# Kernel tuning notes

Hardware: AMD Instinct MI355X
Metric: run time of the kernel (lower is better)

The kernel has to match this reference:

```python
import jax, jax.numpy as jnp
import numpy as np

N_NODES = 40000
N_EDGES = 640000
EMB = 128
OUT_EMB = 256
NUM_DENSE = 3
NUM_TARGETS = 12
NUM_RADIAL = 6


def setup_inputs() -> dict:
    key = jax.random.key(0)
    ks = jax.random.split(key, 8)
    n_atoms = jax.random.normal(ks[0], (N_NODES, EMB), dtype=jnp.float32)
    x = jax.random.normal(ks[1], (N_EDGES, EMB), dtype=jnp.float32)
    rbf = jax.random.normal(ks[2], (N_EDGES, NUM_RADIAL), dtype=jnp.float32)
    idnb_i = jax.random.randint(ks[3], (N_EDGES,), 0, N_NODES, dtype=jnp.int64 if jax.config.read('jax_enable_x64') else jnp.int32)
    s = 0.05
    W_rbf = jax.random.normal(ks[4], (NUM_RADIAL, EMB), dtype=jnp.float32) * s
    W_up = jax.random.normal(ks[5], (EMB, OUT_EMB), dtype=jnp.float32) * s
    W_mlp = jax.random.normal(ks[6], (NUM_DENSE, OUT_EMB, OUT_EMB), dtype=jnp.float32) * s
    b_mlp = jnp.zeros((NUM_DENSE, OUT_EMB), dtype=jnp.float32)
    W_final = jax.random.normal(ks[7], (OUT_EMB, NUM_TARGETS), dtype=jnp.float32) * s
    return {"n_atoms": n_atoms, "x": x, "rbf": rbf, "idnb_i": idnb_i,
            "W_rbf": W_rbf, "W_up": W_up, "W_mlp": W_mlp, "b_mlp": b_mlp,
            "W_final": W_final}


def reference(n_atoms, x, rbf, idnb_i, W_rbf, W_up, W_mlp, b_mlp, W_final):
    # g = Dense(emb_size, no bias)(rbf): [M, EMB]
    g = rbf @ W_rbf
    # elementwise edge gate
    xe = g * x                                  # [M, EMB]
    # scatter-sum edges -> nodes (pooling_method='sum')
    pooled = jax.ops.segment_sum(xe, idnb_i, num_segments=n_atoms.shape[0])  # [N, EMB]
    # up-projection, no bias
    h = pooled @ W_up                           # [N, OUT_EMB]
    # GraphMLP: num_dense layers, swish activation, with bias
    for i in range(W_mlp.shape[0]):
        h = jax.nn.silu(h @ W_mlp[i] + b_mlp[i])
    # final output projection, no bias
    return h @ W_final                          # [N, NUM_TARGETS]
```

## Files before the change

kernel.cpp:

```cpp
#include <hip/hip_runtime.h>
#include <hip/hip_fp16.h>
#include <math.h>

constexpr int kNodes   = 40000;
constexpr int kEdges   = 640000;
constexpr int kEmb     = 128;
constexpr int kOut     = 256;
constexpr int kTargets = 12;
constexpr int kRadial  = 6;

typedef float        f32x4 __attribute__((ext_vector_type(4)));
typedef unsigned int u32x4 __attribute__((ext_vector_type(4)));

__device__ __forceinline__ unsigned short f2h(float f) {
  return __half_as_ushort(__float2half(f));
}
__device__ __forceinline__ void mfma_f16(f32x4& c, u32x4 a, u32x4 b) {
  asm volatile("v_mfma_f32_16x16x32_f16 %0, %1, %2, %0" : "+v"(c) : "v"(a), "v"(b));
}

__global__ __launch_bounds__(256) void zero_counts(int* __restrict__ c) {
  const int i = blockIdx.x * 256 + threadIdx.x;
  if (i < kNodes) c[i] = 0;
}

__global__ __launch_bounds__(256) void hist_kernel(const int* __restrict__ idnb,
                                                   int* __restrict__ counts) {
  const int e = blockIdx.x * 256 + threadIdx.x;
  if (e < kEdges) atomicAdd(&counts[idnb[e]], 1);
}

__global__ __launch_bounds__(256) void scan_pass1(const int* __restrict__ counts,
                                                  int* __restrict__ bsum) {
  __shared__ int sm[256];
  const int idx = blockIdx.x * 256 + threadIdx.x;
  sm[threadIdx.x] = (idx < kNodes) ? counts[idx] : 0;
  __syncthreads();
  for (int d = 128; d > 0; d >>= 1) {
    if (threadIdx.x < d) sm[threadIdx.x] += sm[threadIdx.x + d];
    __syncthreads();
  }
  if (threadIdx.x == 0) bsum[blockIdx.x] = sm[0];
}

__global__ __launch_bounds__(256) void scan_pass3(const int* __restrict__ counts,
                                                  const int* __restrict__ bsum,
                                                  int* __restrict__ offs,
                                                  int* __restrict__ next,
                                                  int nblk) {
  __shared__ int sm[256];
  __shared__ int base;
  const int t = threadIdx.x;
  sm[t] = (t < nblk && t < (int)blockIdx.x) ? bsum[t] : 0;
  __syncthreads();
  for (int d = 128; d > 0; d >>= 1) {
    if (t < d) sm[t] += sm[t + d];
    __syncthreads();
  }
  if (t == 0) base = sm[0];
  __syncthreads();

  const int idx = blockIdx.x * 256 + t;
  const int v = (idx < kNodes) ? counts[idx] : 0;
  sm[t] = v;
  __syncthreads();
  for (int d = 1; d < 256; d <<= 1) {
    const int xsh = (t >= d) ? sm[t - d] : 0;
    __syncthreads();
    sm[t] += xsh;
    __syncthreads();
  }
  if (idx < kNodes) {
    const int e = base + sm[t] - v;
    offs[idx] = e;
    next[idx] = e;
  }
  if (blockIdx.x == 0 && t == 0) offs[kNodes] = kEdges;
}

__global__ __launch_bounds__(256) void fill_kernel(const int* __restrict__ idnb,
                                                   int* __restrict__ next,
                                                   int* __restrict__ edgeIdx) {
  const int e = blockIdx.x * 256 + threadIdx.x;
  if (e < kEdges) {
    const int p = atomicAdd(&next[idnb[e]], 1);
    edgeIdx[p] = e;
  }
}

__global__ __launch_bounds__(256) void prep_weights(
    const float* __restrict__ Wup, const float* __restrict__ Wmlp,
    const float* __restrict__ Wfin,
    unsigned short* __restrict__ WtUp, unsigned short* __restrict__ WtM,
    unsigned short* __restrict__ WtFin) {
  const int id = blockIdx.x * 256 + threadIdx.x;
  if (id < 256 * 128) {
    const int n = id >> 7, k = id & 127;
    WtUp[id] = f2h(Wup[k * 256 + n]);
    return;
  }
  const int id2 = id - 256 * 128;
  if (id2 < 3 * 256 * 256) {
    const int l = id2 >> 16, rem = id2 & 65535, n = rem >> 8, k = rem & 255;
    WtM[id2] = f2h(Wmlp[l * 65536 + k * 256 + n]);
    return;
  }
  const int id3 = id2 - 3 * 256 * 256;
  if (id3 < 16 * 256) {
    const int n = id3 >> 8, k = id3 & 255;
    WtFin[id3] = (n < kTargets) ? f2h(Wfin[k * kTargets + n]) : (unsigned short)0;
  }
}

__global__ __launch_bounds__(256) void gather_kernel(
    const float* __restrict__ x, const float* __restrict__ rbf,
    const int* __restrict__ offs, const int* __restrict__ edgeIdx,
    const float* __restrict__ W_rbf, unsigned short* __restrict__ pooled) {
  __shared__ float wLds[kRadial * kEmb];
  for (int i = threadIdx.x; i < kRadial * kEmb; i += 256) wLds[i] = W_rbf[i];
  __syncthreads();

  const int sub = threadIdx.x & 31;
  const int n   = blockIdx.x * 8 + (threadIdx.x >> 5);

  float4 w[kRadial];
#pragma unroll
  for (int j = 0; j < kRadial; ++j)
    w[j] = *(const float4*)(wLds + j * kEmb + sub * 4);

  const int beg = offs[n], end = offs[n + 1];
  float4 acc = make_float4(0.f, 0.f, 0.f, 0.f);

  if (beg < end) {
    int e = edgeIdx[beg];
    float4 xv = *(const float4*)(x + (size_t)e * kEmb + sub * 4);
    const float* rr = rbf + (size_t)e * kRadial;
    float2 ra = *(const float2*)(rr);
    float2 rb = *(const float2*)(rr + 2);
    float2 rc = *(const float2*)(rr + 4);

    for (int i = beg; i < end; ++i) {
      float4 xv_n;
      float2 na, nb, nc;
      const bool more = (i + 1 < end);
      if (more) {
        const int en = edgeIdx[i + 1];
        xv_n = *(const float4*)(x + (size_t)en * kEmb + sub * 4);
        const float* rn = rbf + (size_t)en * kRadial;
        na = *(const float2*)(rn);
        nb = *(const float2*)(rn + 2);
        nc = *(const float2*)(rn + 4);
      }
      float4 g;
      g.x = ra.x * w[0].x + ra.y * w[1].x + rb.x * w[2].x + rb.y * w[3].x +
            rc.x * w[4].x + rc.y * w[5].x;
      g.y = ra.x * w[0].y + ra.y * w[1].y + rb.x * w[2].y + rb.y * w[3].y +
            rc.x * w[4].y + rc.y * w[5].y;
      g.z = ra.x * w[0].z + ra.y * w[1].z + rb.x * w[2].z + rb.y * w[3].z +
            rc.x * w[4].z + rc.y * w[5].z;
      g.w = ra.x * w[0].w + ra.y * w[1].w + rb.x * w[2].w + rb.y * w[3].w +
            rc.x * w[4].w + rc.y * w[5].w;
      acc.x += g.x * xv.x;
      acc.y += g.y * xv.y;
      acc.z += g.z * xv.z;
      acc.w += g.w * xv.w;
      if (more) {
        xv = xv_n;
        ra = na; rb = nb; rc = nc;
      }
    }
  }
  ushort4 hv;
  hv.x = f2h(acc.x);
  hv.y = f2h(acc.y);
  hv.z = f2h(acc.z);
  hv.w = f2h(acc.w);
  *(ushort4*)(pooled + (size_t)n * kEmb + sub * 4) = hv;
}

__global__ __launch_bounds__(256) void fused_mlp(
    const unsigned short* __restrict__ pooled,
    const unsigned short* __restrict__ WtUp,
    const unsigned short* __restrict__ WtM,
    const unsigned short* __restrict__ WtFin,
    const float* __restrict__ b_mlp, float* __restrict__ out) {
  __shared__ unsigned short act[64][266];
  __shared__ unsigned short sB[2][256][40];

  const int tid     = threadIdx.x;
  const int rowBase = blockIdx.x * 64;
  const int w    = tid >> 6;
  const int lane = tid & 63;
  const int lrow = lane & 15;
  const int kgrp = lane >> 4;

#pragma unroll
  for (int p = 0; p < 4; ++p) {
    const int q = p * 256 + tid;
    const int r = q >> 4, c = q & 15;
    *(u32x4*)&act[r][c * 8] =
        *(const u32x4*)(pooled + (size_t)(rowBase + r) * kEmb + c * 8);
  }
  __syncthreads();

  for (int l = 0; l < 4; ++l) {
    const int K = (l == 0) ? 128 : 256;
    const int nc = K >> 5;
    const unsigned short* W = (l == 0) ? WtUp : WtM + (size_t)(l - 1) * 65536;

#pragma unroll
    for (int p = 0; p < 4; ++p) {
      const int q = p * 256 + tid;
      const int n = q >> 2, c4 = q & 3;
      *(u32x4*)&sB[0][n][c4 * 8] = *(const u32x4*)(W + (size_t)n * K + c4 * 8);
    }
    __syncthreads();

    f32x4 acc[4][4];
#pragma unroll
    for (int i = 0; i < 4; ++i)
#pragma unroll
      for (int j = 0; j < 4; ++j) acc[i][j] = f32x4{0.f, 0.f, 0.f, 0.f};

    for (int c = 0; c < nc; ++c) {
      if (c + 1 < nc) {
        const int kb = (c + 1) * 32;
#pragma unroll
        for (int p = 0; p < 4; ++p) {
          const int q = p * 256 + tid;
          const int n = q >> 2, c4 = q & 3;
          *(u32x4*)&sB[(c + 1) & 1][n][c4 * 8] =
              *(const u32x4*)(W + (size_t)n * K + kb + c4 * 8);
        }
      }
      u32x4 a[4];
#pragma unroll
      for (int i = 0; i < 4; ++i)
        a[i] = *(const u32x4*)&act[i * 16 + lrow][c * 32 + kgrp * 8];
#pragma unroll
      for (int j = 0; j < 4; ++j) {
        const u32x4 b = *(const u32x4*)&sB[c & 1][w * 64 + j * 16 + lrow][kgrp * 8];
#pragma unroll
        for (int i = 0; i < 4; ++i) mfma_f16(acc[i][j], a[i], b);
      }
      __syncthreads();
    }

    const float* bias = (l >= 1) ? b_mlp + (size_t)(l - 1) * kOut : nullptr;
#pragma unroll
    for (int j = 0; j < 4; ++j) {
      const int col = w * 64 + j * 16 + lrow;
      const float bj = (l >= 1) ? bias[col] : 0.f;
#pragma unroll
      for (int i = 0; i < 4; ++i) {
#pragma unroll
        for (int r = 0; r < 4; ++r) {
          float v = acc[i][j][r];
          if (l >= 1) {
            v += bj;
            v = v / (1.f + __expf(-v));
          }
          act[i * 16 + kgrp * 4 + r][col] = f2h(v);
        }
      }
    }
    __syncthreads();
  }

  unsigned short (*sWf)[266] = (unsigned short(*)[266]) & sB[0][0][0];
  float (*sPart)[64][17]     = (float(*)[64][17]) & sB[1][0][0];
#pragma unroll
  for (int p = 0; p < 2; ++p) {
    const int q = p * 256 + tid;
    const int n = q >> 5, c = q & 31;
    *(u32x4*)&sWf[n][c * 8] = *(const u32x4*)(WtFin + (size_t)n * 256 + c * 8);
  }
  __syncthreads();

  f32x4 accF[4];
#pragma unroll
  for (int i = 0; i < 4; ++i) accF[i] = f32x4{0.f, 0.f, 0.f, 0.f};
#pragma unroll
  for (int s = 0; s < 2; ++s) {
    const int cc = w * 2 + s;
    const u32x4 b = *(const u32x4*)&sWf[lrow][cc * 32 + kgrp * 8];
#pragma unroll
    for (int i = 0; i < 4; ++i) {
      const u32x4 a = *(const u32x4*)&act[i * 16 + lrow][cc * 32 + kgrp * 8];
      mfma_f16(accF[i], a, b);
    }
  }
#pragma unroll
  for (int i = 0; i < 4; ++i)
#pragma unroll
    for (int r = 0; r < 4; ++r)
      sPart[w][i * 16 + kgrp * 4 + r][lrow] = accF[i][r];
  __syncthreads();

  for (int q = tid; q < 64 * kTargets; q += 256) {
    const int r = q / kTargets, t = q % kTargets;
    out[(size_t)(rowBase + r) * kTargets + t] =
        sPart[0][r][t] + sPart[1][r][t] + sPart[2][r][t] + sPart[3][r][t];
  }
}

extern "C" void kernel_launch(void* const* d_in, const int* in_sizes, int n_in,
                              void* d_out, int out_size, void* d_ws, size_t ws_size,
                              hipStream_t stream) {
  const float* x      = (const float*)d_in[1];
  const float* rbf    = (const float*)d_in[2];
  const int*   idnb   = (const int*)d_in[3];
  const float* W_rbf  = (const float*)d_in[4];
  const float* W_up   = (const float*)d_in[5];
  const float* W_mlp  = (const float*)d_in[6];
  const float* b_mlp  = (const float*)d_in[7];
  const float* W_fin  = (const float*)d_in[8];
  float* out = (float*)d_out;

  char* wp = (char*)d_ws;
  auto alloc = [&](size_t bytes) -> void* {
    void* r = wp;
    wp += (bytes + 255) & ~(size_t)255;
    return r;
  };
  unsigned short* pooled = (unsigned short*)alloc((size_t)kNodes * kEmb * 2);
  unsigned short* WtUp   = (unsigned short*)alloc(256 * 128 * 2);
  unsigned short* WtM    = (unsigned short*)alloc(3 * 256 * 256 * 2);
  unsigned short* WtFin  = (unsigned short*)alloc(16 * 256 * 2);
  int* counts  = (int*)alloc((size_t)kNodes * 4);
  int* offs    = (int*)alloc((size_t)(kNodes + 8) * 4);
  int* next    = (int*)alloc((size_t)kNodes * 4);
  int* edgeIdx = (int*)alloc((size_t)kEdges * 4);
  int* bsum    = (int*)alloc(256 * 4);

  constexpr int nScanBlk = (kNodes + 255) / 256;

  zero_counts<<<nScanBlk, 256, 0, stream>>>(counts);
  hist_kernel<<<kEdges / 256, 256, 0, stream>>>(idnb, counts);
  scan_pass1<<<nScanBlk, 256, 0, stream>>>(counts, bsum);
  scan_pass3<<<nScanBlk, 256, 0, stream>>>(counts, bsum, offs, next, nScanBlk);
  fill_kernel<<<kEdges / 256, 256, 0, stream>>>(idnb, next, edgeIdx);

  constexpr int prepElems = 256 * 128 + 3 * 256 * 256 + 16 * 256;
  prep_weights<<<(prepElems + 255) / 256, 256, 0, stream>>>(
      W_up, W_mlp, W_fin, WtUp, WtM, WtFin);

  gather_kernel<<<kNodes / 8, 256, 0, stream>>>(x, rbf, offs, edgeIdx, W_rbf,
                                                pooled);

  fused_mlp<<<kNodes / 64, 256, 0, stream>>>(pooled, WtUp, WtM, WtFin, b_mlp,
                                             out);
}
```

Measured before the change: 243.5 us.

## Pre-swizzle MLP weights for direct global-to-LDS loads and fold zeroing into prep

Result: faster. 221.2 us (-9.2%).

```diff
diff --git a/kernel.cpp b/kernel.cpp
--- a/kernel.cpp
+++ b/kernel.cpp
@@ -12,16 +12,14 @@
 typedef float        f32x4 __attribute__((ext_vector_type(4)));
 typedef unsigned int u32x4 __attribute__((ext_vector_type(4)));
 
+typedef __attribute__((address_space(1))) const void gvoid;
+typedef __attribute__((address_space(3))) void       lvoid;
+
 __device__ __forceinline__ unsigned short f2h(float f) {
   return __half_as_ushort(__float2half(f));
 }
 __device__ __forceinline__ void mfma_f16(f32x4& c, u32x4 a, u32x4 b) {
   asm volatile("v_mfma_f32_16x16x32_f16 %0, %1, %2, %0" : "+v"(c) : "v"(a), "v"(b));
-}
-
-__global__ __launch_bounds__(256) void zero_counts(int* __restrict__ c) {
-  const int i = blockIdx.x * 256 + threadIdx.x;
-  if (i < kNodes) c[i] = 0;
 }
 
 __global__ __launch_bounds__(256) void hist_kernel(const int* __restrict__ idnb,
@@ -92,20 +90,29 @@
     const float* __restrict__ Wup, const float* __restrict__ Wmlp,
     const float* __restrict__ Wfin,
     unsigned short* __restrict__ WtUp, unsigned short* __restrict__ WtM,
-    unsigned short* __restrict__ WtFin) {
+    unsigned short* __restrict__ WtFin, int* __restrict__ counts) {
   const int id = blockIdx.x * 256 + threadIdx.x;
-  if (id < 256 * 128) {
-    const int n = id >> 7, k = id & 127;
+  if (id < kNodes) counts[id] = 0;
+
+  if (id < 32768) {
+    const int e = id & 7, u = id >> 3;
+    const int l = u & 63, j = (u >> 6) & 3, wv = (u >> 8) & 3, c = u >> 10;
+    const int n = wv * 64 + j * 16 + (l & 15);
+    const int k = c * 32 + (l >> 4) * 8 + e;
     WtUp[id] = f2h(Wup[k * 256 + n]);
     return;
   }
-  const int id2 = id - 256 * 128;
-  if (id2 < 3 * 256 * 256) {
-    const int l = id2 >> 16, rem = id2 & 65535, n = rem >> 8, k = rem & 255;
-    WtM[id2] = f2h(Wmlp[l * 65536 + k * 256 + n]);
+  const int id2 = id - 32768;
+  if (id2 < 3 * 65536) {
+    const int L = id2 >> 16, r = id2 & 65535;
+    const int e = r & 7, u = r >> 3;
+    const int l = u & 63, j = (u >> 6) & 3, wv = (u >> 8) & 3, c = u >> 10;
+    const int n = wv * 64 + j * 16 + (l & 15);
+    const int k = c * 32 + (l >> 4) * 8 + e;
+    WtM[id2] = f2h(Wmlp[L * 65536 + k * 256 + n]);
     return;
   }
-  const int id3 = id2 - 3 * 256 * 256;
+  const int id3 = id2 - 3 * 65536;
   if (id3 < 16 * 256) {
     const int n = id3 >> 8, k = id3 & 255;
     WtFin[id3] = (n < kTargets) ? f2h(Wfin[k * kTargets + n]) : (unsigned short)0;
@@ -123,52 +130,24 @@
   const int sub = threadIdx.x & 31;
   const int n   = blockIdx.x * 8 + (threadIdx.x >> 5);
 
-  float4 w[kRadial];
+  f32x4 w[kRadial];
 #pragma unroll
   for (int j = 0; j < kRadial; ++j)
-    w[j] = *(const float4*)(wLds + j * kEmb + sub * 4);
+    w[j] = *(const f32x4*)(wLds + j * kEmb + sub * 4);
 
   const int beg = offs[n], end = offs[n + 1];
-  float4 acc = make_float4(0.f, 0.f, 0.f, 0.f);
-
-  if (beg < end) {
-    int e = edgeIdx[beg];
-    float4 xv = *(const float4*)(x + (size_t)e * kEmb + sub * 4);
+  f32x4 acc = {0.f, 0.f, 0.f, 0.f};
+
+  for (int i = beg; i < end; ++i) {
+    const int e = edgeIdx[i];
     const float* rr = rbf + (size_t)e * kRadial;
-    float2 ra = *(const float2*)(rr);
-    float2 rb = *(const float2*)(rr + 2);
-    float2 rc = *(const float2*)(rr + 4);
-
-    for (int i = beg; i < end; ++i) {
-      float4 xv_n;
-      float2 na, nb, nc;
-      const bool more = (i + 1 < end);
-      if (more) {
-        const int en = edgeIdx[i + 1];
-        xv_n = *(const float4*)(x + (size_t)en * kEmb + sub * 4);
-        const float* rn = rbf + (size_t)en * kRadial;
-        na = *(const float2*)(rn);
-        nb = *(const float2*)(rn + 2);
-        nc = *(const float2*)(rn + 4);
-      }
-      float4 g;
-      g.x = ra.x * w[0].x + ra.y * w[1].x + rb.x * w[2].x + rb.y * w[3].x +
-            rc.x * w[4].x + rc.y * w[5].x;
-      g.y = ra.x * w[0].y + ra.y * w[1].y + rb.x * w[2].y + rb.y * w[3].y +
-            rc.x * w[4].y + rc.y * w[5].y;
-      g.z = ra.x * w[0].z + ra.y * w[1].z + rb.x * w[2].z + rb.y * w[3].z +
-            rc.x * w[4].z + rc.y * w[5].z;
-      g.w = ra.x * w[0].w + ra.y * w[1].w + rb.x * w[2].w + rb.y * w[3].w +
-            rc.x * w[4].w + rc.y * w[5].w;
-      acc.x += g.x * xv.x;
-      acc.y += g.y * xv.y;
-      acc.z += g.z * xv.z;
-      acc.w += g.w * xv.w;
-      if (more) {
-        xv = xv_n;
-        ra = na; rb = nb; rc = nc;
-      }
-    }
+    const float r0 = rr[0], r1 = rr[1], r2 = rr[2];
+    const float r3 = rr[3], r4 = rr[4], r5 = rr[5];
+    const f32x4 xv =
+        __builtin_nontemporal_load((const f32x4*)(x + (size_t)e * kEmb + sub * 4));
+    const f32x4 g = r0 * w[0] + r1 * w[1] + r2 * w[2] +
+                    r3 * w[3] + r4 * w[4] + r5 * w[5];
+    acc += g * xv;
   }
   ushort4 hv;
   hv.x = f2h(acc.x);
@@ -185,7 +164,7 @@
     const unsigned short* __restrict__ WtFin,
     const float* __restrict__ b_mlp, float* __restrict__ out) {
   __shared__ unsigned short act[64][266];
-  __shared__ unsigned short sB[2][256][40];
+  __shared__ unsigned short sB[2][8192];
 
   const int tid     = threadIdx.x;
   const int rowBase = blockIdx.x * 64;
@@ -204,17 +183,22 @@
   __syncthreads();
 
   for (int l = 0; l < 4; ++l) {
-    const int K = (l == 0) ? 128 : 256;
-    const int nc = K >> 5;
+    const int nc = (l == 0) ? 4 : 8;
     const unsigned short* W = (l == 0) ? WtUp : WtM + (size_t)(l - 1) * 65536;
 
-#pragma unroll
-    for (int p = 0; p < 4; ++p) {
-      const int q = p * 256 + tid;
-      const int n = q >> 2, c4 = q & 3;
-      *(u32x4*)&sB[0][n][c4 * 8] = *(const u32x4*)(W + (size_t)n * K + c4 * 8);
+    float bj[4] = {0.f, 0.f, 0.f, 0.f};
+    if (l >= 1) {
+      const float* bias = b_mlp + (size_t)(l - 1) * kOut;
+#pragma unroll
+      for (int j = 0; j < 4; ++j) bj[j] = bias[w * 64 + j * 16 + lrow];
+      asm volatile("" ::"v"(bj[0]), "v"(bj[1]), "v"(bj[2]), "v"(bj[3]));
     }
-    __syncthreads();
+
+#pragma unroll
+    for (int j = 0; j < 4; ++j)
+      __builtin_amdgcn_global_load_lds(
+          (gvoid*)(W + w * 2048 + j * 512 + lane * 8),
+          (lvoid*)&sB[0][w * 2048 + j * 512], 16, 0, 0);
 
     f32x4 acc[4][4];
 #pragma unroll
@@ -222,42 +206,46 @@
 #pragma unroll
       for (int j = 0; j < 4; ++j) acc[i][j] = f32x4{0.f, 0.f, 0.f, 0.f};
 
+    int buf = 0;
     for (int c = 0; c < nc; ++c) {
       if (c + 1 < nc) {
-        const int kb = (c + 1) * 32;
-#pragma unroll
-        for (int p = 0; p < 4; ++p) {
-          const int q = p * 256 + tid;
-          const int n = q >> 2, c4 = q & 3;
-          *(u32x4*)&sB[(c + 1) & 1][n][c4 * 8] =
-              *(const u32x4*)(W + (size_t)n * K + kb + c4 * 8);
-        }
+        const unsigned short* Wn = W + (size_t)(c + 1) * 8192;
+#pragma unroll
+        for (int j = 0; j < 4; ++j)
+          __builtin_amdgcn_global_load_lds(
+              (gvoid*)(Wn + w * 2048 + j * 512 + lane * 8),
+              (lvoid*)&sB[buf ^ 1][w * 2048 + j * 512], 16, 0, 0);
+        asm volatile("s_waitcnt vmcnt(4)" ::: "memory");
+      } else {
+        asm volatile("s_waitcnt vmcnt(0)" ::: "memory");
       }
-      u32x4 a[4];
+      u32x4 a[4], b[4];
 #pragma unroll
       for (int i = 0; i < 4; ++i)
         a[i] = *(const u32x4*)&act[i * 16 + lrow][c * 32 + kgrp * 8];
 #pragma unroll
-      for (int j = 0; j < 4; ++j) {
-        const u32x4 b = *(const u32x4*)&sB[c & 1][w * 64 + j * 16 + lrow][kgrp * 8];
-#pragma unroll
-        for (int i = 0; i < 4; ++i) mfma_f16(acc[i][j], a[i], b);
-      }
-      __syncthreads();
+      for (int j = 0; j < 4; ++j)
+        b[j] = *(const u32x4*)&sB[buf][w * 2048 + j * 512 + lane * 8];
+      __builtin_amdgcn_s_setprio(1);
+#pragma unroll
+      for (int j = 0; j < 4; ++j)
+#pragma unroll
+        for (int i = 0; i < 4; ++i) mfma_f16(acc[i][j], a[i], b[j]);
+      __builtin_amdgcn_s_setprio(0);
+      buf ^= 1;
     }
 
-    const float* bias = (l >= 1) ? b_mlp + (size_t)(l - 1) * kOut : nullptr;
+    __syncthreads();
 #pragma unroll
     for (int j = 0; j < 4; ++j) {
       const int col = w * 64 + j * 16 + lrow;
-      const float bj = (l >= 1) ? bias[col] : 0.f;
 #pragma unroll
       for (int i = 0; i < 4; ++i) {
 #pragma unroll
         for (int r = 0; r < 4; ++r) {
           float v = acc[i][j][r];
           if (l >= 1) {
-            v += bj;
+            v += bj[j];
             v = v / (1.f + __expf(-v));
           }
           act[i * 16 + kgrp * 4 + r][col] = f2h(v);
@@ -267,8 +255,8 @@
     __syncthreads();
   }
 
-  unsigned short (*sWf)[266] = (unsigned short(*)[266]) & sB[0][0][0];
-  float (*sPart)[64][17]     = (float(*)[64][17]) & sB[1][0][0];
+  unsigned short (*sWf)[266] = (unsigned short(*)[266]) & sB[0][0];
+  float (*sPart)[64][16]     = (float(*)[64][16]) & sB[1][0];
 #pragma unroll
   for (int p = 0; p < 2; ++p) {
     const int q = p * 256 + tid;
@@ -324,8 +312,8 @@
     return r;
   };
   unsigned short* pooled = (unsigned short*)alloc((size_t)kNodes * kEmb * 2);
-  unsigned short* WtUp   = (unsigned short*)alloc(256 * 128 * 2);
-  unsigned short* WtM    = (unsigned short*)alloc(3 * 256 * 256 * 2);
+  unsigned short* WtUp   = (unsigned short*)alloc(32768 * 2);
+  unsigned short* WtM    = (unsigned short*)alloc(3 * 65536 * 2);
   unsigned short* WtFin  = (unsigned short*)alloc(16 * 256 * 2);
   int* counts  = (int*)alloc((size_t)kNodes * 4);
   int* offs    = (int*)alloc((size_t)(kNodes + 8) * 4);
@@ -334,17 +322,16 @@
   int* bsum    = (int*)alloc(256 * 4);
 
   constexpr int nScanBlk = (kNodes + 255) / 256;
-
-  zero_counts<<<nScanBlk, 256, 0, stream>>>(counts);
+  constexpr int prepElems = 32768 + 3 * 65536 + 16 * 256;
+
+  prep_weights<<<(prepElems + 255) / 256, 256, 0, stream>>>(
+      W_up, W_mlp, W_fin, WtUp, WtM, WtFin, counts);
+
   hist_kernel<<<kEdges / 256, 256, 0, stream>>>(idnb, counts);
   scan_pass1<<<nScanBlk, 256, 0, stream>>>(counts, bsum);
   scan_pass3<<<nScanBlk, 256, 0, stream>>>(counts, bsum, offs, next, nScanBlk);
   fill_kernel<<<kEdges / 256, 256, 0, stream>>>(idnb, next, edgeIdx);
 
-  constexpr int prepElems = 256 * 128 + 3 * 256 * 256 + 16 * 256;
-  prep_weights<<<(prepElems + 255) / 256, 256, 0, stream>>>(
-      W_up, W_mlp, W_fin, WtUp, WtM, WtFin);
-
   gather_kernel<<<kNodes / 8, 256, 0, stream>>>(x, rbf, offs, edgeIdx, W_rbf,
                                                 pooled);
 
```
